# Kernel tuning notes

Hardware: AMD Instinct MI355X
Metric: run time of the kernel (lower is better)

The kernel has to match this reference:

```python
import jax, jax.numpy as jnp
import numpy as np

N = 2048        # number of entities
D = 2048        # entity_dimensionality
HEADS = 16
HD = D // HEADS  # per-head dim = 128
ROUNDS = 2
LAYERS = 2


def setup_inputs() -> dict:
    key = jax.random.key(0)
    ks = jax.random.split(key, 12)
    s = 1.0 / np.sqrt(D)  # keep activations O(1)
    inp = {
        "entities": jax.random.normal(ks[0], (N, D), jnp.float32),
        "Wq": jax.random.normal(ks[1], (D, D), jnp.float32) * s,
        "bq": jnp.zeros((D,), jnp.float32),
        "Wk": jax.random.normal(ks[2], (D, D), jnp.float32) * s,
        "bk": jnp.zeros((D,), jnp.float32),
        "Wv": jax.random.normal(ks[3], (D, D), jnp.float32) * s,
        "bv": jnp.zeros((D,), jnp.float32),
        "W0": jax.random.normal(ks[4], (D, D), jnp.float32) * s,
        "b0": jnp.zeros((D,), jnp.float32),
        "W1": jax.random.normal(ks[5], (D, D), jnp.float32) * s,
        "b1": jnp.zeros((D,), jnp.float32),
    }
    return inp


def _linear(x, W, b):
    # torch nn.Linear: y = x @ W.T + b
    return x @ W.T + b


def _split_heads(x):
    # [N, D] -> [H, N, hd]
    return x.reshape(N, HEADS, HD).transpose(1, 0, 2)


def reference(entities, Wq, bq, Wk, bk, Wv, bv, W0, b0, W1, b1):
    scale = 1.0 / np.sqrt(HD)
    for _ in range(ROUNDS):
        q = _split_heads(_linear(entities, Wq, bq))  # [H, N, hd]
        k = _split_heads(_linear(entities, Wk, bk))
        v = _split_heads(_linear(entities, Wv, bv))
        scores = jnp.einsum('hqd,hkd->hqk', q, k) * scale  # [H, N, N]
        attn = jax.nn.softmax(scores, axis=-1)
        o = jnp.einsum('hqk,hkd->hqd', attn, v)            # [H, N, hd]
        o = o.transpose(1, 0, 2).reshape(N, D)             # merge heads
        o = jax.nn.relu(_linear(o, W0, b0))
        o = jax.nn.relu(_linear(o, W1, b1))
        entities = entities + o  # residual=True
    return entities
```

## Files before the change

### kernel.cpp

```cpp
#include <hip/hip_runtime.h>
#include <stdint.h>

#define DIM   2048
#define NENT  2048
#define NHEAD 16
#define HD    128

typedef unsigned short u16;
typedef u16   u16x4  __attribute__((ext_vector_type(4)));
typedef u16   u16x8  __attribute__((ext_vector_type(8)));
typedef float f32x4  __attribute__((ext_vector_type(4)));
typedef float f32x16 __attribute__((ext_vector_type(16)));
typedef __bf16 bf16x8 __attribute__((ext_vector_type(8)));

#define MFMA16(a, b, c) __builtin_amdgcn_mfma_f32_16x16x32_bf16((a), (b), (c), 0, 0, 0)
#define MFMA32(a, b, c) __builtin_amdgcn_mfma_f32_32x32x16_bf16((a), (b), (c), 0, 0, 0)

#define SMUL 0.12751743f

__device__ __forceinline__ u16 f2b(float f) {
  union { float f; unsigned int u; } x; x.f = f;
  unsigned int r = x.u + 0x7FFFu + ((x.u >> 16) & 1u);
  return (u16)(r >> 16);
}
__device__ __forceinline__ float b2f(u16 b) {
  union { unsigned int u; float f; } x; x.u = ((unsigned int)b) << 16;
  return x.f;
}
__device__ __forceinline__ unsigned int cvtpk(float a, float b) {
  unsigned int r;
  asm("v_cvt_pk_bf16_f32 %0, %1, %2" : "=v"(r) : "v"(a), "v"(b));
  return r;
}
__device__ __forceinline__ float exp2_fast(float x) {
  float r;
  asm("v_exp_f32 %0, %1" : "=v"(r) : "v"(x));
  return r;
}

__device__ __forceinline__ void async16(const void* g, void* l) {
  __builtin_amdgcn_global_load_lds(
      (const __attribute__((address_space(1))) unsigned int*)(uintptr_t)g,
      (__attribute__((address_space(3))) unsigned int*)(uintptr_t)l, 16, 0, 0);
}

__global__ void __launch_bounds__(256) conv6_k(
    const float* __restrict__ s0, const float* __restrict__ s1,
    const float* __restrict__ s2, const float* __restrict__ s3,
    const float* __restrict__ s4, const float* __restrict__ s5,
    u16* __restrict__ d0, u16* __restrict__ d1, u16* __restrict__ d2,
    u16* __restrict__ d3, u16* __restrict__ d4, u16* __restrict__ d5) {
  int sel = blockIdx.y;
  const float* s = sel == 0 ? s0 : sel == 1 ? s1 : sel == 2 ? s2
                 : sel == 3 ? s3 : sel == 4 ? s4 : s5;
  u16* d = sel == 0 ? d0 : sel == 1 ? d1 : sel == 2 ? d2
         : sel == 3 ? d3 : sel == 4 ? d4 : d5;
  int i = blockIdx.x * 256 + threadIdx.x;
  float4 v = ((const float4*)s)[i];
  u16x4 o;
  o.x = f2b(v.x); o.y = f2b(v.y); o.z = f2b(v.z); o.w = f2b(v.w);
  *(u16x4*)(d + (size_t)i * 4) = o;
}

template <int MODE, int NT>
__device__ __forceinline__ void gemm256_body(
    const u16* __restrict__ A, const u16* __restrict__ Bw,
    const float* __restrict__ bias, u16* __restrict__ C,
    int brow0, int bcol0, int kbase, float oscale) {
  __shared__ u16 lds[2][4][128 * 64];
  const int tid = threadIdx.x;
  const int lane = tid & 63, w = tid >> 6;
  const int wr = w >> 2, wc = w & 3;
  const int l15 = lane & 15;
  const int koff = (lane >> 4) * 8;
  const int swz = (l15 & 7) << 3;

  f32x4 acc[8][4];
#pragma unroll
  for (int m = 0; m < 8; m++)
#pragma unroll
    for (int n = 0; n < 4; n++) acc[m][n] = (f32x4)0.f;

  const int srow = lane >> 3;
  const int scol = ((lane & 7) ^ srow) * 8;

  auto stageTile = [&](int kt) {
    const int slot = kt & 1;
    const int colg = kbase + kt * 64 + scol;
    const u16* Ab = A + (size_t)(brow0 + w * 16 + srow) * DIM + colg;
    const u16* Bb = Bw + (size_t)(bcol0 + w * 16 + srow) * DIM + colg;
    u16* d0 = &lds[slot][0][w * 1024];
    u16* d1 = &lds[slot][1][w * 1024];
    u16* d2 = &lds[slot][2][w * 1024];
    u16* d3 = &lds[slot][3][w * 1024];
    async16(Ab, d0);
    async16(Ab + 8 * DIM, d0 + 512);
    async16(Ab + 128 * DIM, d1);
    async16(Ab + 136 * DIM, d1 + 512);
    async16(Bb, d2);
    async16(Bb + 8 * DIM, d2 + 512);
    async16(Bb + 128 * DIM, d3);
    async16(Bb + 136 * DIM, d3 + 512);
  };

  stageTile(0);

#pragma unroll 1
  for (int kt = 0; kt < NT; kt++) {
    const int slot = kt & 1;
    const u16* Ah = &lds[slot][wr][0];
    const u16* Bh = &lds[slot][2 + (wc >> 1)][0];
    const int brw = (wc & 1) * 64;

    if (kt + 1 < NT) {
      stageTile(kt + 1);
      asm volatile("s_waitcnt vmcnt(8)" ::: "memory");
    } else {
      asm volatile("s_waitcnt vmcnt(0)" ::: "memory");
    }
    __builtin_amdgcn_s_barrier();

    bf16x8 bfr[4];
#pragma unroll
    for (int kk = 0; kk < 2; kk++) {
#pragma unroll
      for (int mh = 0; mh < 2; mh++) {
        if (mh == 0) {
#pragma unroll
          for (int n = 0; n < 4; n++)
            bfr[n] = *(const bf16x8*)(Bh + (brw + n * 16 + l15) * 64 +
                                      ((kk * 32 + koff) ^ swz));
        }
        bf16x8 af[4];
#pragma unroll
        for (int m = 0; m < 4; m++)
          af[m] = *(const bf16x8*)(Ah + (mh * 64 + m * 16 + l15) * 64 +
                                   ((kk * 32 + koff) ^ swz));
        __builtin_amdgcn_s_barrier();
        __builtin_amdgcn_s_setprio(1);
#pragma unroll
        for (int m = 0; m < 4; m++)
#pragma unroll
          for (int n = 0; n < 4; n++)
            acc[mh * 4 + m][n] = MFMA16(af[m], bfr[n], acc[mh * 4 + m][n]);
        __builtin_amdgcn_s_setprio(0);
        __builtin_amdgcn_s_barrier();
      }
    }
  }

#pragma unroll
  for (int n = 0; n < 4; n++) {
    int col = bcol0 + wc * 64 + n * 16 + l15;
    float bv = (MODE == 0) ? bias[col] : 0.f;
#pragma unroll
    for (int m = 0; m < 8; m++) {
#pragma unroll
      for (int r = 0; r < 4; r++) {
        int row = brow0 + wr * 128 + m * 16 + (lane >> 4) * 4 + r;
        float val = acc[m][n][r] + bv;
        if (MODE == 0) val *= oscale;
        C[(size_t)row * DIM + col] = f2b(val);
      }
    }
  }
}

__global__ void __launch_bounds__(512, 2) gemm256_qkv_k(
    const u16* __restrict__ A,
    const u16* __restrict__ Bq, const u16* __restrict__ Bk, const u16* __restrict__ Bv,
    const float* __restrict__ bq, const float* __restrict__ bk, const float* __restrict__ bv,
    u16* __restrict__ q, u16* __restrict__ k, u16* __restrict__ v) {
  int id = (blockIdx.x % 8) * 24 + blockIdx.x / 8;
  int bm = id / 24, idn = id % 24;
  int sel = idn >> 3, bn = idn & 7;
  const u16* B = sel == 0 ? Bq : (sel == 1 ? Bk : Bv);
  const float* bias = sel == 0 ? bq : (sel == 1 ? bk : bv);
  u16* C = sel == 0 ? q : (sel == 1 ? k : v);
  gemm256_body<0, 32>(A, B, bias, C, bm * 256, bn * 256, 0,
                      sel == 0 ? SMUL : 1.f);
}

__global__ void __launch_bounds__(512, 2) gemm256_sk_k(
    const u16* __restrict__ A, const u16* __restrict__ Bw,
    u16* __restrict__ p0, u16* __restrict__ p1,
    u16* __restrict__ p2, u16* __restrict__ p3) {
  int id = (blockIdx.x % 8) * 32 + blockIdx.x / 8;
  int bn = id & 7, sk = (id >> 3) & 3, bm = id >> 5;
  u16* part = sk == 0 ? p0 : (sk == 1 ? p1 : (sk == 2 ? p2 : p3));
  gemm256_body<1, 8>(A, Bw, nullptr, part, bm * 256, bn * 256, sk * 512, 1.f);
}

template <int RESID>
__global__ void __launch_bounds__(256) reduce4_k(
    const u16* __restrict__ p0, const u16* __restrict__ p1,
    const u16* __restrict__ p2, const u16* __restrict__ p3,
    const float* __restrict__ bias, const float* __restrict__ resid,
    float* __restrict__ outf, u16* __restrict__ outb) {
  int i = blockIdx.x * 256 + threadIdx.x;
  u16x8 a0 = ((const u16x8*)p0)[i];
  u16x8 a1 = ((const u16x8*)p1)[i];
  u16x8 a2 = ((const u16x8*)p2)[i];
  u16x8 a3 = ((const u16x8*)p3)[i];
  size_t base = (size_t)i * 8;
  int col = (int)(base & (DIM - 1));
  u16x8 ob;
  float of[8];
#pragma unroll
  for (int j = 0; j < 8; j++) {
    float s = b2f(a0[j]) + b2f(a1[j]) + b2f(a2[j]) + b2f(a3[j]) + bias[col + j];
    s = fmaxf(s, 0.f);
    if (RESID) {
      float o = resid[base + j] + s;
      of[j] = o;
      ob[j] = f2b(o);
    } else {
      ob[j] = f2b(s);
    }
  }
  *(u16x8*)(outb + base) = ob;
  if (RESID) {
#pragma unroll
    for (int j = 0; j < 8; j++) outf[base + j] = of[j];
  }
}

__global__ void __launch_bounds__(256) transpose_v_k(const u16* __restrict__ v,
                                                     u16* __restrict__ vt) {
  __shared__ u16 t[64][72];
  int h = blockIdx.z, nb = blockIdx.y, db = blockIdx.x;
  int tid = threadIdx.x;
  int r0 = tid >> 3, c0 = (tid & 7) * 8;
#pragma unroll
  for (int p = 0; p < 2; p++) {
    int r = r0 + p * 32;
    const u16* src = v + (size_t)(nb * 64 + r) * DIM + h * HD + db * 64 + c0;
    u16x8 x = *(const u16x8*)src;
#pragma unroll
    for (int j = 0; j < 8; j++) t[r][c0 + j] = x[j];
  }
  __syncthreads();
#pragma unroll
  for (int p = 0; p < 2; p++) {
    int rr = r0 + p * 32;
    u16x8 x;
#pragma unroll
    for (int j = 0; j < 8; j++) x[j] = t[c0 + j][rr];
    *(u16x8*)(vt + (size_t)h * HD * NENT + (size_t)(db * 64 + rr) * NENT + nb * 64 + c0) = x;
  }
}

__global__ void __launch_bounds__(256, 2) attn_k(
    const u16* __restrict__ q, const u16* __restrict__ kmat,
    const u16* __restrict__ vt, u16* __restrict__ oz0, u16* __restrict__ oz1,
    float* __restrict__ ml) {
  const int h = blockIdx.x, qb = blockIdx.y, kvs = blockIdx.z;
  u16* __restrict__ oz = kvs ? oz1 : oz0;
  __shared__ u16 lK[2][64 * 128];
  __shared__ u16 lV[2][128 * 64];
  const int tid = threadIdx.x, lane = tid & 63, w = tid >> 6;
  const int l31 = lane & 31, hl = lane >> 5;
  const int r4 = lane >> 4, r8 = lane >> 3;
  const int c16e = (lane & 15) * 8, c8e = (lane & 7) * 8;
  const int swz = (l31 & 7) << 3;
  const u16* vhead = vt + (size_t)h * HD * NENT;
  const int kv0 = kvs * (NENT / 2);

  const int qrow = qb * 128 + w * 32 + l31;
  const u16* qptr = q + (size_t)qrow * DIM + h * HD + hl * 8;
  bf16x8 qf[8];
#pragma unroll
  for (int ks = 0; ks < 8; ks++)
    qf[ks] = *(const bf16x8*)(qptr + ks * 16);

  auto stageKV = [&](int kt, int buf) {
    const size_t krow0 = (size_t)kv0 + kt * 64;
#pragma unroll
    for (int c = 0; c < 4; c++) {
      int ch = w * 4 + c;
      int krow = ch * 4 + r4;
      async16(kmat + (krow0 + krow) * DIM + h * HD + (c16e ^ ((krow & 7) << 3)),
              lK[buf] + ch * 512);
      int vrow = ch * 8 + r8;
      async16(vhead + (size_t)vrow * NENT + krow0 + (c8e ^ ((r8 & 7) << 3)),
              lV[buf] + ch * 512);
    }
  };

  f32x16 Oacc[4];
#pragma unroll
  for (int dt = 0; dt < 4; dt++) Oacc[dt] = (f32x16)0.f;
  float m_i = -1e30f, l_i = 0.f;

  stageKV(0, 0);
  int cur = 0;

#pragma unroll 1
  for (int kt = 0; kt < NENT / 2 / 64; kt++) {
    __syncthreads();
    if (kt + 1 < NENT / 2 / 64) stageKV(kt + 1, cur ^ 1);
    const u16* Kc = lK[cur];
    const u16* Vc = lV[cur];

    f32x16 sA = (f32x16)0.f, sB = (f32x16)0.f;
#pragma unroll
    for (int ks = 0; ks < 8; ks++) {
      bf16x8 a0 = *(const bf16x8*)(Kc + l31 * 128 + ((ks * 16 + hl * 8) ^ swz));
      sA = MFMA32(a0, qf[ks], sA);
      bf16x8 a1 = *(const bf16x8*)(Kc + (32 + l31) * 128 + ((ks * 16 + hl * 8) ^ swz));
      sB = MFMA32(a1, qf[ks], sB);
    }

    float pmax = sA[0];
#pragma unroll
    for (int i = 1; i < 16; i++) pmax = fmaxf(pmax, sA[i]);
#pragma unroll
    for (int i = 0; i < 16; i++) pmax = fmaxf(pmax, sB[i]);
    pmax = fmaxf(pmax, __shfl_xor(pmax, 32));
    bool resc = __any(pmax > m_i + 8.f);
    float corr = 1.f;
    if (resc) {
      float mn = fmaxf(m_i, pmax);
      corr = exp2_fast(m_i - mn);
      m_i = mn;
    }
    float ls = 0.f;
#pragma unroll
    for (int i = 0; i < 16; i++) { sA[i] = exp2_fast(sA[i] - m_i); ls += sA[i]; }
#pragma unroll
    for (int i = 0; i < 16; i++) { sB[i] = exp2_fast(sB[i] - m_i); ls += sB[i]; }
    l_i = l_i * corr + ls;
    if (resc) {
#pragma unroll
      for (int r = 0; r < 16; r++) {
        int qo = hl * 4 + (r & 3) + 8 * (r >> 2);
        float cr = __shfl(corr, qo);
        Oacc[0][r] *= cr; Oacc[1][r] *= cr; Oacc[2][r] *= cr; Oacc[3][r] *= cr;
      }
    }

#pragma unroll
    for (int ks = 0; ks < 4; ks++) {
      const f32x16& p = (ks < 2) ? sA : sB;
      const int E = ((2 * ks) & 3) * 4;
      const int Od = ((2 * ks + 1) & 3) * 4;
      unsigned int e0 = cvtpk(p[E + 0], p[E + 1]);
      unsigned int e1 = cvtpk(p[E + 2], p[E + 3]);
      unsigned int o0 = cvtpk(p[Od + 0], p[Od + 1]);
      unsigned int o1 = cvtpk(p[Od + 2], p[Od + 3]);
      asm volatile("v_permlane32_swap_b32 %0, %1" : "+v"(e0), "+v"(o0));
      asm volatile("v_permlane32_swap_b32 %0, %1" : "+v"(e1), "+v"(o1));
      union { unsigned int u[4]; bf16x8 v; } pk;
      pk.u[0] = e0; pk.u[1] = e1; pk.u[2] = o0; pk.u[3] = o1;
#pragma unroll
      for (int dt = 0; dt < 4; dt++) {
        bf16x8 b = *(const bf16x8*)(Vc + (dt * 32 + l31) * 64 +
                                    ((ks * 16 + hl * 8) ^ swz));
        Oacc[dt] = MFMA32(pk.v, b, Oacc[dt]);
      }
    }
    cur ^= 1;
  }

  float lt = l_i + __shfl_xor(l_i, 32);
  if (hl == 0) {
    float* mlp = ml + ((size_t)(kvs * NHEAD + h) * NENT + qrow) * 2;
    mlp[0] = m_i;
    mlp[1] = lt;
  }
#pragma unroll
  for (int r = 0; r < 16; r++) {
    int row = qb * 128 + w * 32 + hl * 4 + (r & 3) + 8 * (r >> 2);
#pragma unroll
    for (int dt = 0; dt < 4; dt++)
      oz[(size_t)row * DIM + h * HD + dt * 32 + l31] = f2b(Oacc[dt][r]);
  }
}

__global__ void __launch_bounds__(256) combine_k(
    const u16* __restrict__ O0, const u16* __restrict__ O1,
    const float* __restrict__ ml, u16* __restrict__ o) {
  int i = blockIdx.x * 256 + threadIdx.x;
  size_t base = (size_t)i * 8;
  int row = (int)(base >> 11);
  int h = ((int)base & (DIM - 1)) >> 7;
  const float* p0 = ml + ((size_t)h * NENT + row) * 2;
  const float* p1 = ml + ((size_t)(NHEAD + h) * NENT + row) * 2;
  float m0 = p0[0], l0 = p0[1];
  float m1 = p1[0], l1 = p1[1];
  float M = fmaxf(m0, m1);
  float w0 = exp2_fast(m0 - M), w1 = exp2_fast(m1 - M);
  float inv = 1.f / (l0 * w0 + l1 * w1);
  w0 *= inv; w1 *= inv;
  u16x8 a = ((const u16x8*)O0)[i], b = ((const u16x8*)O1)[i];
  u16x8 r;
#pragma unroll
  for (int j = 0; j < 8; j++) r[j] = f2b(b2f(a[j]) * w0 + b2f(b[j]) * w1);
  ((u16x8*)o)[i] = r;
}

extern "C" void kernel_launch(void* const* d_in, const int* in_sizes, int n_in,
                              void* d_out, int out_size, void* d_ws, size_t ws_size,
                              hipStream_t stream) {
  const float* ent_in = (const float*)d_in[0];
  const float* Wq = (const float*)d_in[1];
  const float* bq = (const float*)d_in[2];
  const float* Wk = (const float*)d_in[3];
  const float* bk = (const float*)d_in[4];
  const float* Wv = (const float*)d_in[5];
  const float* bv = (const float*)d_in[6];
  const float* W0 = (const float*)d_in[7];
  const float* b0 = (const float*)d_in[8];
  const float* W1 = (const float*)d_in[9];
  const float* b1 = (const float*)d_in[10];
  float* out = (float*)d_out;

  char* ws = (char*)d_ws;
  const size_t SZ = (size_t)DIM * DIM * 2;
  u16* wqb = (u16*)ws; ws += SZ;
  u16* wkb = (u16*)ws; ws += SZ;
  u16* wvb = (u16*)ws; ws += SZ;
  u16* w0b = (u16*)ws; ws += SZ;
  u16* w1b = (u16*)ws; ws += SZ;
  u16* entb = (u16*)ws; ws += SZ;
  u16* qb_ = (u16*)ws; ws += SZ;
  u16* kb_ = (u16*)ws; ws += SZ;
  u16* vb_ = (u16*)ws; ws += SZ;
  u16* vtb = (u16*)ws; ws += SZ;
  u16* ob_ = (u16*)ws; ws += SZ;
  u16* h1b = (u16*)ws; ws += SZ;

  conv6_k<<<dim3(4096, 6), 256, 0, stream>>>(Wq, Wk, Wv, W0, W1, ent_in,
                                             wqb, wkb, wvb, w0b, w1b, entb);

  for (int r = 0; r < 2; r++) {
    const float* cur = r ? (const float*)out : ent_in;
    gemm256_qkv_k<<<192, 512, 0, stream>>>(entb, wqb, wkb, wvb, bq, bk, bv,
                                           qb_, kb_, vb_);
    transpose_v_k<<<dim3(2, 32, 16), 256, 0, stream>>>(vb_, vtb);
    attn_k<<<dim3(16, 16, 2), 256, 0, stream>>>(qb_, kb_, vtb, vb_, h1b,
                                                (float*)entb);
    combine_k<<<2048, 256, 0, stream>>>(vb_, h1b, (const float*)entb, ob_);
    gemm256_sk_k<<<256, 512, 0, stream>>>(ob_, w0b, entb, qb_, kb_, vb_);
    reduce4_k<0><<<2048, 256, 0, stream>>>(entb, qb_, kb_, vb_, b0, nullptr,
                                           nullptr, h1b);
    gemm256_sk_k<<<256, 512, 0, stream>>>(h1b, w1b, entb, qb_, kb_, vb_);
    reduce4_k<1><<<2048, 256, 0, stream>>>(entb, qb_, kb_, vb_, b1, cur,
                                           out, entb);
  }
}
```

Before: 413.0 us.

## Replace 256x256 double-buffered GEMM with simpler 128x128 tiles and 2-way split-K

The GEMM kernels move from 256x256 tiles with 512 threads, double-buffered async LDS staging and priority/barrier interleaving to 128x128 tiles with 256 threads and a single LDS buffer synchronised by __syncthreads. The MLP GEMMs now split K two ways instead of four, so the reduce kernels read two partial buffers instead of four. This gives more blocks for occupancy and less partial-sum traffic, but drops load/compute overlap and lowers per-block data reuse.

Result: no change. 419.9 us (+1.7%).

```diff
diff --git a/kernel.cpp b/kernel.cpp
--- a/kernel.cpp
+++ b/kernel.cpp
@@ -63,90 +63,57 @@
 }
 
 template <int MODE, int NT>
-__device__ __forceinline__ void gemm256_body(
+__device__ __forceinline__ void gemm128_body(
     const u16* __restrict__ A, const u16* __restrict__ Bw,
     const float* __restrict__ bias, u16* __restrict__ C,
     int brow0, int bcol0, int kbase, float oscale) {
-  __shared__ u16 lds[2][4][128 * 64];
+  __shared__ u16 lA[128 * 64];
+  __shared__ u16 lB[128 * 64];
   const int tid = threadIdx.x;
   const int lane = tid & 63, w = tid >> 6;
-  const int wr = w >> 2, wc = w & 3;
+  const int wr = w >> 1, wc = w & 1;
   const int l15 = lane & 15;
   const int koff = (lane >> 4) * 8;
   const int swz = (l15 & 7) << 3;
 
-  f32x4 acc[8][4];
-#pragma unroll
-  for (int m = 0; m < 8; m++)
+  f32x4 acc[4][4];
+#pragma unroll
+  for (int m = 0; m < 4; m++)
 #pragma unroll
     for (int n = 0; n < 4; n++) acc[m][n] = (f32x4)0.f;
 
-  const int srow = lane >> 3;
-  const int scol = ((lane & 7) ^ srow) * 8;
-
-  auto stageTile = [&](int kt) {
-    const int slot = kt & 1;
-    const int colg = kbase + kt * 64 + scol;
-    const u16* Ab = A + (size_t)(brow0 + w * 16 + srow) * DIM + colg;
-    const u16* Bb = Bw + (size_t)(bcol0 + w * 16 + srow) * DIM + colg;
-    u16* d0 = &lds[slot][0][w * 1024];
-    u16* d1 = &lds[slot][1][w * 1024];
-    u16* d2 = &lds[slot][2][w * 1024];
-    u16* d3 = &lds[slot][3][w * 1024];
-    async16(Ab, d0);
-    async16(Ab + 8 * DIM, d0 + 512);
-    async16(Ab + 128 * DIM, d1);
-    async16(Ab + 136 * DIM, d1 + 512);
-    async16(Bb, d2);
-    async16(Bb + 8 * DIM, d2 + 512);
-    async16(Bb + 128 * DIM, d3);
-    async16(Bb + 136 * DIM, d3 + 512);
-  };
-
-  stageTile(0);
+  const int lr = w * 8 + (lane >> 3);
+  const int scol = ((lane & 7) ^ (lr & 7)) * 8;
 
 #pragma unroll 1
   for (int kt = 0; kt < NT; kt++) {
-    const int slot = kt & 1;
-    const u16* Ah = &lds[slot][wr][0];
-    const u16* Bh = &lds[slot][2 + (wc >> 1)][0];
-    const int brw = (wc & 1) * 64;
-
-    if (kt + 1 < NT) {
-      stageTile(kt + 1);
-      asm volatile("s_waitcnt vmcnt(8)" ::: "memory");
-    } else {
-      asm volatile("s_waitcnt vmcnt(0)" ::: "memory");
-    }
-    __builtin_amdgcn_s_barrier();
-
-    bf16x8 bfr[4];
+    const int colg = kbase + kt * 64 + scol;
+#pragma unroll
+    for (int i = 0; i < 4; i++) {
+      async16(A + (size_t)(brow0 + i * 32 + lr) * DIM + colg,
+              lA + i * 2048 + w * 512);
+      async16(Bw + (size_t)(bcol0 + i * 32 + lr) * DIM + colg,
+              lB + i * 2048 + w * 512);
+    }
+    __syncthreads();
 #pragma unroll
     for (int kk = 0; kk < 2; kk++) {
-#pragma unroll
-      for (int mh = 0; mh < 2; mh++) {
-        if (mh == 0) {
-#pragma unroll
-          for (int n = 0; n < 4; n++)
-            bfr[n] = *(const bf16x8*)(Bh + (brw + n * 16 + l15) * 64 +
-                                      ((kk * 32 + koff) ^ swz));
-        }
-        bf16x8 af[4];
-#pragma unroll
-        for (int m = 0; m < 4; m++)
-          af[m] = *(const bf16x8*)(Ah + (mh * 64 + m * 16 + l15) * 64 +
-                                   ((kk * 32 + koff) ^ swz));
-        __builtin_amdgcn_s_barrier();
-        __builtin_amdgcn_s_setprio(1);
-#pragma unroll
-        for (int m = 0; m < 4; m++)
-#pragma unroll
-          for (int n = 0; n < 4; n++)
-            acc[mh * 4 + m][n] = MFMA16(af[m], bfr[n], acc[mh * 4 + m][n]);
-        __builtin_amdgcn_s_setprio(0);
-        __builtin_amdgcn_s_barrier();
-      }
-    }
+      bf16x8 af[4], bfr[4];
+#pragma unroll
+      for (int m = 0; m < 4; m++)
+        af[m] = *(const bf16x8*)(lA + (wr * 64 + m * 16 + l15) * 64 +
+                                 ((kk * 32 + koff) ^ swz));
+#pragma unroll
+      for (int n = 0; n < 4; n++)
+        bfr[n] = *(const bf16x8*)(lB + (wc * 64 + n * 16 + l15) * 64 +
+                                  ((kk * 32 + koff) ^ swz));
+#pragma unroll
+      for (int m = 0; m < 4; m++)
+#pragma unroll
+        for (int n = 0; n < 4; n++)
+          acc[m][n] = MFMA16(af[m], bfr[n], acc[m][n]);
+    }
+    __syncthreads();
   }
 
 #pragma unroll
@@ -154,10 +121,10 @@
     int col = bcol0 + wc * 64 + n * 16 + l15;
     float bv = (MODE == 0) ? bias[col] : 0.f;
 #pragma unroll
-    for (int m = 0; m < 8; m++) {
+    for (int m = 0; m < 4; m++) {
 #pragma unroll
       for (int r = 0; r < 4; r++) {
-        int row = brow0 + wr * 128 + m * 16 + (lane >> 4) * 4 + r;
+        int row = brow0 + wr * 64 + m * 16 + (lane >> 4) * 4 + r;
         float val = acc[m][n][r] + bv;
         if (MODE == 0) val *= oscale;
         C[(size_t)row * DIM + col] = f2b(val);
@@ -166,49 +133,47 @@
   }
 }
 
-__global__ void __launch_bounds__(512, 2) gemm256_qkv_k(
+__global__ void __launch_bounds__(256) gemm128_qkv_k(
     const u16* __restrict__ A,
     const u16* __restrict__ Bq, const u16* __restrict__ Bk, const u16* __restrict__ Bv,
     const float* __restrict__ bq, const float* __restrict__ bk, const float* __restrict__ bv,
     u16* __restrict__ q, u16* __restrict__ k, u16* __restrict__ v) {
-  int id = (blockIdx.x % 8) * 24 + blockIdx.x / 8;
-  int bm = id / 24, idn = id % 24;
-  int sel = idn >> 3, bn = idn & 7;
+  int bid = blockIdx.x;
+  int id = (bid & 7) * 96 + (bid >> 3);
+  int bm = id / 48, bn = id % 48;
+  int sel = bn >> 4, bnn = bn & 15;
   const u16* B = sel == 0 ? Bq : (sel == 1 ? Bk : Bv);
   const float* bias = sel == 0 ? bq : (sel == 1 ? bk : bv);
-  u16* C = sel == 0 ? q : (sel == 1 ? k : v);
-  gemm256_body<0, 32>(A, B, bias, C, bm * 256, bn * 256, 0,
+  u16* Cc = sel == 0 ? q : (sel == 1 ? k : v);
+  gemm128_body<0, 32>(A, B, bias, Cc, bm * 128, bnn * 128, 0,
                       sel == 0 ? SMUL : 1.f);
 }
 
-__global__ void __launch_bounds__(512, 2) gemm256_sk_k(
+__global__ void __launch_bounds__(256) gemm128_sk_k(
     const u16* __restrict__ A, const u16* __restrict__ Bw,
-    u16* __restrict__ p0, u16* __restrict__ p1,
-    u16* __restrict__ p2, u16* __restrict__ p3) {
-  int id = (blockIdx.x % 8) * 32 + blockIdx.x / 8;
-  int bn = id & 7, sk = (id >> 3) & 3, bm = id >> 5;
-  u16* part = sk == 0 ? p0 : (sk == 1 ? p1 : (sk == 2 ? p2 : p3));
-  gemm256_body<1, 8>(A, Bw, nullptr, part, bm * 256, bn * 256, sk * 512, 1.f);
+    u16* __restrict__ p0, u16* __restrict__ p1) {
+  int bid = blockIdx.x;
+  int id = (bid & 7) * 64 + (bid >> 3);
+  int bn = id & 15, sk = (id >> 4) & 1, bm = id >> 5;
+  u16* part = sk ? p1 : p0;
+  gemm128_body<1, 16>(A, Bw, nullptr, part, bm * 128, bn * 128, sk * 1024, 1.f);
 }
 
 template <int RESID>
-__global__ void __launch_bounds__(256) reduce4_k(
+__global__ void __launch_bounds__(256) reduce2_k(
     const u16* __restrict__ p0, const u16* __restrict__ p1,
-    const u16* __restrict__ p2, const u16* __restrict__ p3,
     const float* __restrict__ bias, const float* __restrict__ resid,
     float* __restrict__ outf, u16* __restrict__ outb) {
   int i = blockIdx.x * 256 + threadIdx.x;
   u16x8 a0 = ((const u16x8*)p0)[i];
   u16x8 a1 = ((const u16x8*)p1)[i];
-  u16x8 a2 = ((const u16x8*)p2)[i];
-  u16x8 a3 = ((const u16x8*)p3)[i];
   size_t base = (size_t)i * 8;
   int col = (int)(base & (DIM - 1));
   u16x8 ob;
   float of[8];
 #pragma unroll
   for (int j = 0; j < 8; j++) {
-    float s = b2f(a0[j]) + b2f(a1[j]) + b2f(a2[j]) + b2f(a3[j]) + bias[col + j];
+    float s = b2f(a0[j]) + b2f(a1[j]) + bias[col + j];
     s = fmaxf(s, 0.f);
     if (RESID) {
       float o = resid[base + j] + s;
@@ -435,17 +400,17 @@
 
   for (int r = 0; r < 2; r++) {
     const float* cur = r ? (const float*)out : ent_in;
-    gemm256_qkv_k<<<192, 512, 0, stream>>>(entb, wqb, wkb, wvb, bq, bk, bv,
+    gemm128_qkv_k<<<768, 256, 0, stream>>>(entb, wqb, wkb, wvb, bq, bk, bv,
                                            qb_, kb_, vb_);
     transpose_v_k<<<dim3(2, 32, 16), 256, 0, stream>>>(vb_, vtb);
     attn_k<<<dim3(16, 16, 2), 256, 0, stream>>>(qb_, kb_, vtb, vb_, h1b,
                                                 (float*)entb);
     combine_k<<<2048, 256, 0, stream>>>(vb_, h1b, (const float*)entb, ob_);
-    gemm256_sk_k<<<256, 512, 0, stream>>>(ob_, w0b, entb, qb_, kb_, vb_);
-    reduce4_k<0><<<2048, 256, 0, stream>>>(entb, qb_, kb_, vb_, b0, nullptr,
+    gemm128_sk_k<<<512, 256, 0, stream>>>(ob_, w0b, entb, qb_);
+    reduce2_k<0><<<2048, 256, 0, stream>>>(entb, qb_, b0, nullptr,
                                            nullptr, h1b);
-    gemm256_sk_k<<<256, 512, 0, stream>>>(h1b, w1b, entb, qb_, kb_, vb_);
-    reduce4_k<1><<<2048, 256, 0, stream>>>(entb, qb_, kb_, vb_, b1, cur,
+    gemm128_sk_k<<<512, 256, 0, stream>>>(h1b, w1b, entb, qb_);
+    reduce2_k<1><<<2048, 256, 0, stream>>>(entb, qb_, b1, cur,
                                            out, entb);
   }
 }
```
